# Optimization experiments

Measured on AMD Instinct MI355X. Metric: run time of the kernel, lower is better.

Reference implementation:

```python
import jax, jax.numpy as jnp
import numpy as np

D_IN = 1024
D_OUT = 1024
NUM_HEADS = 16
HEAD_DIM = D_OUT // NUM_HEADS


def setup_inputs() -> dict:
    key = jax.random.key(0)
    k_x, k_q, k_k, k_v, k_o, k_ob = jax.random.split(key, 6)
    s_in = 1.0 / np.sqrt(D_IN)
    s_out = 1.0 / np.sqrt(D_OUT)
    return {
        "x": jax.random.normal(k_x, (4, 2048, D_IN), dtype=jnp.float32),
        "W_Q": jax.random.uniform(k_q, (D_IN, D_OUT), jnp.float32, -s_in, s_in),
        "W_K": jax.random.uniform(k_k, (D_IN, D_OUT), jnp.float32, -s_in, s_in),
        "W_V": jax.random.uniform(k_v, (D_IN, D_OUT), jnp.float32, -s_in, s_in),
        "W_O": jax.random.uniform(k_o, (D_OUT, D_OUT), jnp.float32, -s_out, s_out),
        "b_O": jax.random.uniform(k_ob, (D_OUT,), jnp.float32, -s_out, s_out),
    }


def reference(x, W_Q, W_K, W_V, W_O, b_O):
    B, T, _ = x.shape
    # projections -> [B, H, T, Dh]
    Q = (x @ W_Q).reshape(B, T, NUM_HEADS, HEAD_DIM).transpose(0, 2, 1, 3)
    K = (x @ W_K).reshape(B, T, NUM_HEADS, HEAD_DIM).transpose(0, 2, 1, 3)
    V = (x @ W_V).reshape(B, T, NUM_HEADS, HEAD_DIM).transpose(0, 2, 1, 3)
    scores = jnp.einsum("bhqd,bhkd->bhqk", Q, K) / np.sqrt(HEAD_DIM).astype(np.float32)
    causal = jnp.tril(jnp.ones((T, T), dtype=bool))  # True = keep
    scores = jnp.where(causal, scores, -jnp.inf)
    weights = jax.nn.softmax(scores, axis=-1)
    ctx = jnp.einsum("bhqk,bhkd->bhqd", weights, V)
    ctx = ctx.transpose(0, 2, 1, 3).reshape(B, T, D_OUT)
    return ctx @ W_O + b_O
```

## Files before the change

### kernel.cpp

```cpp
#include <hip/hip_runtime.h>

typedef unsigned short ushort_t;
typedef __attribute__((ext_vector_type(8))) __bf16 bf16x8;
typedef __attribute__((ext_vector_type(4))) float f32x4;
typedef __attribute__((ext_vector_type(16))) float f32x16;
typedef __attribute__((ext_vector_type(4))) unsigned short us4;
typedef __attribute__((ext_vector_type(8))) unsigned short us8;
typedef __attribute__((ext_vector_type(4))) unsigned int u32x4;

#define AS1 __attribute__((address_space(1)))
#define AS3 __attribute__((address_space(3)))

__device__ __forceinline__ unsigned short f2bf(float f) {
    unsigned u = __float_as_uint(f);
    u += 0x7fff + ((u >> 16) & 1);
    return (unsigned short)(u >> 16);
}

__device__ __forceinline__ unsigned cvtpk_bf16(float lo, float hi) {
    unsigned r;
    asm("v_cvt_pk_bf16_f32 %0, %1, %2" : "=v"(r) : "v"(lo), "v"(hi));
    return r;
}

__device__ __forceinline__ float fast_exp2(float x) {
    float r;
    asm("v_exp_f32 %0, %1" : "=v"(r) : "v"(x));
    return r;
}

__global__ void k_convert_x(const float* __restrict__ x, ushort_t* __restrict__ xb, int n4) {
    int i = blockIdx.x * blockDim.x + threadIdx.x;
    int stride = gridDim.x * blockDim.x;
    for (; i < n4; i += stride) {
        float4 f = reinterpret_cast<const float4*>(x)[i];
        us4 o = { f2bf(f.x), f2bf(f.y), f2bf(f.z), f2bf(f.w) };
        reinterpret_cast<us4*>(xb)[i] = o;
    }
}

__global__ void k_transpose_w(const float* __restrict__ wq, const float* __restrict__ wk,
                              const float* __restrict__ wv, const float* __restrict__ wo,
                              ushort_t* __restrict__ wqkvt, ushort_t* __restrict__ wot) {
    __shared__ float t[64][65];
    int bx = blockIdx.x;
    int w = bx >> 8;
    int ti = bx & 255;
    int k0 = (ti >> 4) * 64, n0 = (ti & 15) * 64;
    const float* src = (w == 0) ? wq : (w == 1) ? wk : (w == 2) ? wv : wo;
    ushort_t* dst = (w < 3) ? (wqkvt + (size_t)w * 1048576) : wot;
    for (int i = threadIdx.x; i < 4096; i += 256) {
        int r = i >> 6, c = i & 63;
        t[c][r] = src[(size_t)(k0 + r) * 1024 + n0 + c];
    }
    __syncthreads();
    for (int i = threadIdx.x; i < 4096; i += 256) {
        int r = i >> 6, c = i & 63;
        dst[(size_t)(n0 + r) * 1024 + k0 + c] = f2bf(t[r][c]);
    }
}

__global__ __launch_bounds__(512, 2) void k_gemm_qkv256(
    const ushort_t* __restrict__ A, const ushort_t* __restrict__ Bm,
    ushort_t* __restrict__ qd, ushort_t* __restrict__ kd, ushort_t* __restrict__ vtd) {
    __shared__ __attribute__((aligned(16))) ushort_t lds[2 * 28672];

    const int tid = threadIdx.x, wid = tid >> 6, lane = tid & 63;
    const int lr = lane & 15, lg = lane >> 4;
    const int wm = wid >> 2, wn = wid & 3;

    int bid = blockIdx.x;
    int wg = (bid & 7) * 64 + (bid >> 3);
    const int by = wg >> 4, bx = wg & 15;
    const int row0 = by * 256, col0 = bx * 192;

    const int srcrow = lane >> 2;
    const int srccol = (((lane & 3) * 16) ^ ((lane >> 5) << 5)) >> 1;
    const ushort_t* aS = A  + (size_t)(row0 + srcrow) * 1024 + srccol;
    const ushort_t* bS = Bm + (size_t)(col0 + srcrow) * 1024 + srccol;
    const int rdoff = (lr * 64 + lg * 16) ^ ((lr >> 3) << 5);

    const int s0 = (wid & 3) + ((wid >> 2) << 3);
    const int s1 = s0 + 4;
    const int bmix_sr = 8 + (wid & 3);
    const int bmix_sc = wid >> 2;

#define STG_A(kt, sr, sc) \
    __builtin_amdgcn_global_load_lds((const AS1 void*)(aS + (size_t)(sr) * 16384 + (kt) * 64 + (sc) * 32), \
        (AS3 void*)((AS3 char*)lds + ((kt) & 1) * 57344 + (sr) * 2048 + (sc) * 1024), 16, 0, 0)
#define STG_B(kt, sr, sc) \
    __builtin_amdgcn_global_load_lds((const AS1 void*)(bS + (size_t)(sr) * 16384 + (kt) * 64 + (sc) * 32), \
        (AS3 void*)((AS3 char*)lds + ((kt) & 1) * 57344 + 32768 + (sr) * 2048 + (sc) * 1024), 16, 0, 0)
#define GRP1(kt)  { STG_A(kt, s0, 0); STG_B(kt, wid, 0); }
#define GRP2(kt)  { STG_A(kt, s1, 0); }
#define GRP3(kt)  { STG_A(kt, s0, 1); STG_B(kt, wid, 1); }
#define GTOP(kt)  { STG_A(kt, s1, 1); STG_B(kt, bmix_sr, bmix_sc); }

    f32x4 acc[8][3] = {};

    GRP1(0); GRP2(0); GRP3(0); GTOP(0);
    GRP1(1); GRP2(1); GRP3(1);

#pragma unroll 1
    for (int kt = 0; kt < 16; ++kt) {
        if (kt < 15) asm volatile("s_waitcnt vmcnt(5)" ::: "memory");
        else         asm volatile("s_waitcnt vmcnt(0)" ::: "memory");
        __builtin_amdgcn_s_barrier();
        if (kt < 15) GTOP(kt + 1);

        const char* bufA = (const char*)lds + (kt & 1) * 57344;
        const char* bufB = bufA + 32768;

        bf16x8 av0[4], av1[4], bv0[3], bv1[3];
#pragma unroll
        for (int x = 0; x < 4; ++x)
            av0[x] = *reinterpret_cast<const bf16x8*>(bufA + (wm * 8 + x) * 2048 + rdoff);
#pragma unroll
        for (int x = 0; x < 3; ++x)
            bv0[x] = *reinterpret_cast<const bf16x8*>(bufB + (wn * 3 + x) * 2048 + rdoff);

#pragma unroll
        for (int x = 0; x < 4; ++x)
            av1[x] = *reinterpret_cast<const bf16x8*>(bufA + (wm * 8 + 4 + x) * 2048 + rdoff);
        __builtin_amdgcn_s_setprio(1);
#pragma unroll
        for (int mf = 0; mf < 4; ++mf)
#pragma unroll
            for (int nf = 0; nf < 3; ++nf)
                acc[mf][nf] = __builtin_amdgcn_mfma_f32_16x16x32_bf16(av0[mf], bv0[nf], acc[mf][nf], 0, 0, 0);
        __builtin_amdgcn_s_setprio(0);
        __builtin_amdgcn_s_barrier();

#pragma unroll
        for (int x = 0; x < 4; ++x)
            av0[x] = *reinterpret_cast<const bf16x8*>(bufA + (wm * 8 + x) * 2048 + 1024 + rdoff);
#pragma unroll
        for (int x = 0; x < 3; ++x)
            bv1[x] = *reinterpret_cast<const bf16x8*>(bufB + (wn * 3 + x) * 2048 + 1024 + rdoff);
        __builtin_amdgcn_s_setprio(1);
#pragma unroll
        for (int mf = 0; mf < 4; ++mf)
#pragma unroll
            for (int nf = 0; nf < 3; ++nf)
                acc[4 + mf][nf] = __builtin_amdgcn_mfma_f32_16x16x32_bf16(av1[mf], bv0[nf], acc[4 + mf][nf], 0, 0, 0);
        __builtin_amdgcn_s_setprio(0);
        if (kt < 14) GRP1(kt + 2);
        __builtin_amdgcn_s_barrier();

#pragma unroll
        for (int x = 0; x < 4; ++x)
            av1[x] = *reinterpret_cast<const bf16x8*>(bufA + (wm * 8 + 4 + x) * 2048 + 1024 + rdoff);
        __builtin_amdgcn_s_setprio(1);
#pragma unroll
        for (int mf = 0; mf < 4; ++mf)
#pragma unroll
            for (int nf = 0; nf < 3; ++nf)
                acc[mf][nf] = __builtin_amdgcn_mfma_f32_16x16x32_bf16(av0[mf], bv1[nf], acc[mf][nf], 0, 0, 0);
        __builtin_amdgcn_s_setprio(0);
        if (kt < 14) GRP2(kt + 2);
        __builtin_amdgcn_s_barrier();

        __builtin_amdgcn_s_setprio(1);
#pragma unroll
        for (int mf = 0; mf < 4; ++mf)
#pragma unroll
            for (int nf = 0; nf < 3; ++nf)
                acc[4 + mf][nf] = __builtin_amdgcn_mfma_f32_16x16x32_bf16(av1[mf], bv1[nf], acc[4 + mf][nf], 0, 0, 0);
        __builtin_amdgcn_s_setprio(0);
        if (kt < 14) GRP3(kt + 2);
    }
#undef STG_A
#undef STG_B
#undef GRP1
#undef GRP2
#undef GRP3
#undef GTOP

#pragma unroll
    for (int mi = 0; mi < 8; ++mi) {
#pragma unroll
        for (int nf = 0; nf < 3; ++nf) {
            int col = col0 + wn * 48 + nf * 16 + lr;
            int w = col >> 10;
            int c1 = col & 1023;
            int h = c1 >> 6, dh = c1 & 63;
            if (w < 2) {
                ushort_t* dst = (w == 0) ? qd : kd;
                const float osc = (w == 0) ? 0.18033688f : 1.0f;
#pragma unroll
                for (int e = 0; e < 4; ++e) {
                    int row = row0 + wm * 128 + mi * 16 + lg * 4 + e;
                    int b = row >> 11, t = row & 2047;
                    dst[(((size_t)(b * 16 + h)) * 2048 + t) * 64 + dh] = f2bf(acc[mi][nf][e] * osc);
                }
            } else {
                int rbase = row0 + wm * 128 + mi * 16 + lg * 4;
                int b = rbase >> 11, t0 = rbase & 2047;
                us4 o = { f2bf(acc[mi][nf][0]), f2bf(acc[mi][nf][1]),
                          f2bf(acc[mi][nf][2]), f2bf(acc[mi][nf][3]) };
                *reinterpret_cast<us4*>(
                    &vtd[(((size_t)(b * 16 + h)) * 64 + dh) * 2048 + t0]) = o;
            }
        }
    }
}

__global__ __launch_bounds__(256) void k_attn(
    const ushort_t* __restrict__ q, const ushort_t* __restrict__ k,
    const ushort_t* __restrict__ v, ushort_t* __restrict__ ctx) {
    __shared__ __attribute__((aligned(16))) ushort_t lsK[2 * 8192];
    __shared__ __attribute__((aligned(16))) ushort_t lsV[2 * 8192];

    const int tid = threadIdx.x, wid = tid >> 6, lane = tid & 63;
    const int l31 = lane & 31, hi = lane >> 5;
    const int bid = blockIdx.x;
    const int bh = bid & 63, pi = bid >> 6;
    const size_t base = (size_t)bh * 2048 * 64;
    const ushort_t* qg = q + base;
    const ushort_t* kg = k + base;
    const ushort_t* vtg = v + base;
    const int b = bh >> 4, h = bh & 15;

    const int skey = wid * 8 + (lane >> 3);
    const int scb0 = ((lane & 7) * 16) ^ ((skey & 7) << 4);
    const int kx = (l31 & 7) << 4;
    int koffA[4];
#pragma unroll
    for (int s = 0; s < 4; ++s)
        koffA[s] = l31 * 128 + ((s * 32 + hi * 16) ^ kx);

    us8 ow;
#pragma unroll
    for (int e = 0; e < 8; ++e) ow[e] = 0x3F80;
    const bf16x8 onef = __builtin_bit_cast(bf16x8, ow);

#pragma unroll 1
    for (int pass = 0; pass < 2; ++pass) {
        const int qt = pass ? pi : (15 - pi);
        const int q0 = qt * 128;
        const int q0w = q0 + wid * 32;
        const int qrow = q0w + l31;
        const int njt = qt + 1;

        bf16x8 qf[4];
#pragma unroll
        for (int s = 0; s < 4; ++s)
            qf[s] = *reinterpret_cast<const bf16x8*>(qg + (size_t)qrow * 64 + s * 16 + hi * 8);

        const ushort_t* kpr[4];
        const ushort_t* vpr[4];
#pragma unroll
        for (int r = 0; r < 4; ++r) {
            kpr[r] = kg + (size_t)(r * 32 + skey) * 64 + (scb0 >> 1);
            vpr[r] = vtg + (size_t)((r & 1) * 32 + skey) * 2048 + (r >> 1) * 64 + (scb0 >> 1);
        }

        f32x16 acc0 = {}, acc1 = {}, lacc = {};

        __syncthreads();
#pragma unroll
        for (int r = 0; r < 4; ++r) {
            __builtin_amdgcn_global_load_lds((const AS1 void*)kpr[r],
                (AS3 void*)((AS3 char*)lsK + r * 4096 + wid * 1024), 16, 0, 0);
            __builtin_amdgcn_global_load_lds((const AS1 void*)vpr[r],
                (AS3 void*)((AS3 char*)lsV + r * 4096 + wid * 1024), 16, 0, 0);
        }

        unsigned bo = 0;
        for (int jt = 0; jt < njt; ++jt) {
            __syncthreads();
            const int j0 = jt << 7;
            if (jt + 1 < njt) {
                const unsigned nb = bo ^ 16384;
#pragma unroll
                for (int r = 0; r < 4; ++r) {
                    kpr[r] += 8192;
                    vpr[r] += 128;
                    __builtin_amdgcn_global_load_lds((const AS1 void*)kpr[r],
                        (AS3 void*)((AS3 char*)lsK + nb + r * 4096 + wid * 1024), 16, 0, 0);
                    __builtin_amdgcn_global_load_lds((const AS1 void*)vpr[r],
                        (AS3 void*)((AS3 char*)lsV + nb + r * 4096 + wid * 1024), 16, 0, 0);
                }
            }

#pragma unroll
            for (int hh = 0; hh < 2; ++hh) {
                const int j0h = j0 + hh * 64;
                if (j0h < q0w + 32) {
                    const char* bK = reinterpret_cast<const char*>(lsK) + bo + hh * 8192;
                    const char* bV = reinterpret_cast<const char*>(lsV) + bo + hh * 8192;

                    f32x16 s0 = {}, s1 = {};
#pragma unroll
                    for (int s = 0; s < 4; ++s) {
                        bf16x8 ka = *reinterpret_cast<const bf16x8*>(bK + koffA[s]);
                        s0 = __builtin_amdgcn_mfma_f32_32x32x16_bf16(ka, qf[s], s0, 0, 0, 0);
                    }
#pragma unroll
                    for (int s = 0; s < 4; ++s) {
                        bf16x8 ka = *reinterpret_cast<const bf16x8*>(bK + 4096 + koffA[s]);
                        s1 = __builtin_amdgcn_mfma_f32_32x32x16_bf16(ka, qf[s], s1, 0, 0, 0);
                    }

                    float p0[16], p1[16];
                    if (j0h + 63 > q0w) {
                        const int jh = j0h + 4 * hi;
#pragma unroll
                        for (int r = 0; r < 16; ++r) {
                            const int kl = jh + (r & 3) + 8 * (r >> 2);
                            float e0 = fast_exp2(s0[r]);
                            float e1 = fast_exp2(s1[r]);
                            p0[r] = (kl > qrow) ? 0.f : e0;
                            p1[r] = (kl + 32 > qrow) ? 0.f : e1;
                        }
                    } else {
#pragma unroll
                        for (int r = 0; r < 16; ++r) {
                            p0[r] = fast_exp2(s0[r]);
                            p1[r] = fast_exp2(s1[r]);
                        }
                    }

#pragma unroll
                    for (int kb = 0; kb < 2; ++kb) {
                        const float* pp = kb ? p1 : p0;
                        unsigned pw[8];
#pragma unroll
                        for (int g = 0; g < 4; ++g) {
                            pw[2 * g]     = cvtpk_bf16(pp[4 * g],     pp[4 * g + 1]);
                            pw[2 * g + 1] = cvtpk_bf16(pp[4 * g + 2], pp[4 * g + 3]);
                        }
#pragma unroll
                        for (int j = 0; j < 2; ++j) {
                            asm("v_permlane32_swap_b32 %0, %1" : "+v"(pw[4 * j]),     "+v"(pw[4 * j + 2]));
                            asm("v_permlane32_swap_b32 %0, %1" : "+v"(pw[4 * j + 1]), "+v"(pw[4 * j + 3]));
                            u32x4 fw = { pw[4 * j], pw[4 * j + 1], pw[4 * j + 2], pw[4 * j + 3] };
                            bf16x8 pf = __builtin_bit_cast(bf16x8, fw);
                            const int jj = kb * 2 + j;
                            {
                                bf16x8 vf = *reinterpret_cast<const bf16x8*>(bV + koffA[jj]);
                                acc0 = __builtin_amdgcn_mfma_f32_32x32x16_bf16(vf, pf, acc0, 0, 0, 0);
                            }
                            {
                                bf16x8 vf = *reinterpret_cast<const bf16x8*>(bV + 4096 + koffA[jj]);
                                acc1 = __builtin_amdgcn_mfma_f32_32x32x16_bf16(vf, pf, acc1, 0, 0, 0);
                            }
                            lacc = __builtin_amdgcn_mfma_f32_32x32x16_bf16(onef, pf, lacc, 0, 0, 0);
                        }
                    }
                }
            }
            bo ^= 16384;
        }

        float inv = 1.0f / lacc[0];
        size_t orow = ((size_t)(b * 2048 + qrow)) * 1024 + h * 64;
#pragma unroll
        for (int g = 0; g < 4; ++g) {
            us4 o0 = { f2bf(acc0[4 * g] * inv),     f2bf(acc0[4 * g + 1] * inv),
                       f2bf(acc0[4 * g + 2] * inv), f2bf(acc0[4 * g + 3] * inv) };
            *reinterpret_cast<us4*>(&ctx[orow + 8 * g + 4 * hi]) = o0;
            us4 o1 = { f2bf(acc1[4 * g] * inv),     f2bf(acc1[4 * g + 1] * inv),
                       f2bf(acc1[4 * g + 2] * inv), f2bf(acc1[4 * g + 3] * inv) };
            *reinterpret_cast<us4*>(&ctx[orow + 32 + 8 * g + 4 * hi]) = o1;
        }
    }
}

__global__ __launch_bounds__(256, 2) void k_gemm_out(
    const ushort_t* __restrict__ cb, const ushort_t* __restrict__ wot,
    const float* __restrict__ bO, float* __restrict__ out) {
    __shared__ __attribute__((aligned(16))) ushort_t lds[2 * 16384];

    const int tid = threadIdx.x, wid = tid >> 6, lane = tid & 63;
    const int lr = lane & 15, lg = lane >> 4;
    const int wm = wid >> 1, wn = wid & 1;

    int bid = blockIdx.x;
    int wg = (bid & 7) * 64 + (bid >> 3);
    const int by = wg >> 3, bx = wg & 7;
    const int row0 = by * 128, col0 = bx * 128;

    const int srcrow = lane >> 2;
    const int srccol = (((lane & 3) * 16) ^ ((lane >> 5) << 5)) >> 1;
    const ushort_t* aS = cb  + (size_t)(row0 + srcrow) * 1024 + srccol;
    const ushort_t* bS = wot + (size_t)(col0 + srcrow) * 1024 + srccol;
    const int rdoff = (lr * 64 + lg * 16) ^ ((lr >> 3) << 5);

#define STG_A(kt, sr, sc) \
    __builtin_amdgcn_global_load_lds((const AS1 void*)(aS + (size_t)(sr) * 16384 + (kt) * 64 + (sc) * 32), \
        (AS3 void*)((AS3 char*)lds + ((kt) & 1) * 32768 + (sr) * 2048 + (sc) * 1024), 16, 0, 0)
#define STG_B(kt, sr, sc) \
    __builtin_amdgcn_global_load_lds((const AS1 void*)(bS + (size_t)(sr) * 16384 + (kt) * 64 + (sc) * 32), \
        (AS3 void*)((AS3 char*)lds + ((kt) & 1) * 32768 + 16384 + (sr) * 2048 + (sc) * 1024), 16, 0, 0)
#define GRP1(kt)  { STG_A(kt, wid, 0); STG_A(kt, wid + 4, 0); STG_B(kt, wid, 0); STG_B(kt, wid + 4, 0); }
#define GTOP(kt)  { STG_A(kt, wid, 1); STG_A(kt, wid + 4, 1); STG_B(kt, wid, 1); STG_B(kt, wid + 4, 1); }

    f32x4 acc[4][4] = {};

    GRP1(0); GTOP(0); GRP1(1);

#pragma unroll 1
    for (int kt = 0; kt < 16; ++kt) {
        if (kt < 15) asm volatile("s_waitcnt vmcnt(4)" ::: "memory");
        else         asm volatile("s_waitcnt vmcnt(0)" ::: "memory");
        __builtin_amdgcn_s_barrier();
        if (kt < 15) GTOP(kt + 1);

        const char* bufA = (const char*)lds + (kt & 1) * 32768;
        const char* bufB = bufA + 16384;

        bf16x8 av0[2], av1[2], bv0[4], bv1[4];
#pragma unroll
        for (int x = 0; x < 2; ++x)
            av0[x] = *reinterpret_cast<const bf16x8*>(bufA + (wm * 4 + x) * 2048 + rdoff);
#pragma unroll
        for (int x = 0; x < 4; ++x)
            bv0[x] = *reinterpret_cast<const bf16x8*>(bufB + (wn * 4 + x) * 2048 + rdoff);

#pragma unroll
        for (int x = 0; x < 2; ++x)
            av1[x] = *reinterpret_cast<const bf16x8*>(bufA + (wm * 4 + 2 + x) * 2048 + rdoff);
        __builtin_amdgcn_s_setprio(1);
#pragma unroll
        for (int mf = 0; mf < 2; ++mf)
#pragma unroll
            for (int nf = 0; nf < 4; ++nf)
                acc[mf][nf] = __builtin_amdgcn_mfma_f32_16x16x32_bf16(av0[mf], bv0[nf], acc[mf][nf], 0, 0, 0);
        __builtin_amdgcn_s_setprio(0);
        __builtin_amdgcn_s_barrier();

#pragma unroll
        for (int x = 0; x < 2; ++x)
            av0[x] = *reinterpret_cast<const bf16x8*>(bufA + (wm * 4 + x) * 2048 + 1024 + rdoff);
#pragma unroll
        for (int x = 0; x < 4; ++x)
            bv1[x] = *reinterpret_cast<const bf16x8*>(bufB + (wn * 4 + x) * 2048 + 1024 + rdoff);
        __builtin_amdgcn_s_setprio(1);
#pragma unroll
        for (int mf = 0; mf < 2; ++mf)
#pragma unroll
            for (int nf = 0; nf < 4; ++nf)
                acc[2 + mf][nf] = __builtin_amdgcn_mfma_f32_16x16x32_bf16(av1[mf], bv0[nf], acc[2 + mf][nf], 0, 0, 0);
        __builtin_amdgcn_s_setprio(0);
        if (kt < 14) GRP1(kt + 2);
        __builtin_amdgcn_s_barrier();

#pragma unroll
        for (int x = 0; x < 2; ++x)
            av1[x] = *reinterpret_cast<const bf16x8*>(bufA + (wm * 4 + 2 + x) * 2048 + 1024 + rdoff);
        __builtin_amdgcn_s_setprio(1);
#pragma unroll
        for (int mf = 0; mf < 2; ++mf)
#pragma unroll
            for (int nf = 0; nf < 4; ++nf)
                acc[mf][nf] = __builtin_amdgcn_mfma_f32_16x16x32_bf16(av0[mf], bv1[nf], acc[mf][nf], 0, 0, 0);
        __builtin_amdgcn_s_setprio(0);
        __builtin_amdgcn_s_barrier();

        __builtin_amdgcn_s_setprio(1);
#pragma unroll
        for (int mf = 0; mf < 2; ++mf)
#pragma unroll
            for (int nf = 0; nf < 4; ++nf)
                acc[2 + mf][nf] = __builtin_amdgcn_mfma_f32_16x16x32_bf16(av1[mf], bv1[nf], acc[2 + mf][nf], 0, 0, 0);
        __builtin_amdgcn_s_setprio(0);
    }
#undef STG_A
#undef STG_B
#undef GRP1
#undef GTOP

#pragma unroll
    for (int mf = 0; mf < 4; ++mf) {
#pragma unroll
        for (int nf = 0; nf < 4; ++nf) {
            int col = col0 + wn * 64 + nf * 16 + lr;
            float bias = bO[col];
#pragma unroll
            for (int e = 0; e < 4; ++e) {
                int row = row0 + wm * 64 + mf * 16 + lg * 4 + e;
                out[(size_t)row * 1024 + col] = acc[mf][nf][e] + bias;
            }
        }
    }
}

extern "C" void kernel_launch(void* const* d_in, const int* in_sizes, int n_in,
                              void* d_out, int out_size, void* d_ws, size_t ws_size,
                              hipStream_t stream) {
    const float* x  = (const float*)d_in[0];
    const float* wq = (const float*)d_in[1];
    const float* wk = (const float*)d_in[2];
    const float* wv = (const float*)d_in[3];
    const float* wo = (const float*)d_in[4];
    const float* bo = (const float*)d_in[5];
    float* out = (float*)d_out;

    char* ws = (char*)d_ws;
    ushort_t* xb    = (ushort_t*)(ws);
    ushort_t* wqkvt = (ushort_t*)(ws + 16777216);
    ushort_t* wot   = (ushort_t*)(ws + 23068672);
    ushort_t* qd    = (ushort_t*)(ws + 25165824);
    ushort_t* kd    = (ushort_t*)(ws + 41943040);
    ushort_t* vtd   = (ushort_t*)(ws + 58720256);
    ushort_t* cd    = (ushort_t*)(ws + 75497472);

    k_convert_x<<<2048, 256, 0, stream>>>(x, xb, 8192 * 1024 / 4);
    k_transpose_w<<<1024, 256, 0, stream>>>(wq, wk, wv, wo, wqkvt, wot);
    k_gemm_qkv256<<<512, 512, 0, stream>>>(xb, wqkvt, qd, kd, vtd);
    k_attn<<<512, 256, 0, stream>>>(qd, kd, vtd, cd);
    k_gemm_out<<<dim3(512), 256, 0, stream>>>(cd, wot, bo, out);
}
```

Measured before the change: 152.0 us.

## Shrink QKV GEMM tile to 128x192 and double the grid

The QKV projection GEMM moves from 256x192 tiles on 512 blocks to 128x192 tiles on 1024 blocks. LDS per block shrinks and launch bounds are raised to 4 blocks per CU. The k-loop pipeline becomes two MFMA phases with fewer staging groups and a lower vmcnt wait. The aim is more concurrent blocks and better CU balance, at the cost of lower arithmetic intensity per tile and more global reloads of the weight matrix.

```diff
diff --git a/kernel.cpp b/kernel.cpp
--- a/kernel.cpp
+++ b/kernel.cpp
@@ -60,19 +60,19 @@
     }
 }
 
-__global__ __launch_bounds__(512, 2) void k_gemm_qkv256(
+__global__ __launch_bounds__(512, 4) void k_gemm_qkv128(
     const ushort_t* __restrict__ A, const ushort_t* __restrict__ Bm,
     ushort_t* __restrict__ qd, ushort_t* __restrict__ kd, ushort_t* __restrict__ vtd) {
-    __shared__ __attribute__((aligned(16))) ushort_t lds[2 * 28672];
+    __shared__ __attribute__((aligned(16))) ushort_t lds[2 * 20480];
 
     const int tid = threadIdx.x, wid = tid >> 6, lane = tid & 63;
     const int lr = lane & 15, lg = lane >> 4;
     const int wm = wid >> 2, wn = wid & 3;
 
     int bid = blockIdx.x;
-    int wg = (bid & 7) * 64 + (bid >> 3);
+    int wg = (bid & 7) * 128 + (bid >> 3);
     const int by = wg >> 4, bx = wg & 15;
-    const int row0 = by * 256, col0 = bx * 192;
+    const int row0 = by * 128, col0 = bx * 192;
 
     const int srcrow = lane >> 2;
     const int srccol = (((lane & 3) * 16) ^ ((lane >> 5) << 5)) >> 1;
@@ -80,48 +80,44 @@
     const ushort_t* bS = Bm + (size_t)(col0 + srcrow) * 1024 + srccol;
     const int rdoff = (lr * 64 + lg * 16) ^ ((lr >> 3) << 5);
 
-    const int s0 = (wid & 3) + ((wid >> 2) << 3);
-    const int s1 = s0 + 4;
-    const int bmix_sr = 8 + (wid & 3);
-    const int bmix_sc = wid >> 2;
+    const int bx_sr = 8 + (wid & 3);
+    const int bx_sc = wid >> 2;
 
 #define STG_A(kt, sr, sc) \
     __builtin_amdgcn_global_load_lds((const AS1 void*)(aS + (size_t)(sr) * 16384 + (kt) * 64 + (sc) * 32), \
-        (AS3 void*)((AS3 char*)lds + ((kt) & 1) * 57344 + (sr) * 2048 + (sc) * 1024), 16, 0, 0)
+        (AS3 void*)((AS3 char*)lds + ((kt) & 1) * 40960 + (sr) * 2048 + (sc) * 1024), 16, 0, 0)
 #define STG_B(kt, sr, sc) \
     __builtin_amdgcn_global_load_lds((const AS1 void*)(bS + (size_t)(sr) * 16384 + (kt) * 64 + (sc) * 32), \
-        (AS3 void*)((AS3 char*)lds + ((kt) & 1) * 57344 + 32768 + (sr) * 2048 + (sc) * 1024), 16, 0, 0)
-#define GRP1(kt)  { STG_A(kt, s0, 0); STG_B(kt, wid, 0); }
-#define GRP2(kt)  { STG_A(kt, s1, 0); }
-#define GRP3(kt)  { STG_A(kt, s0, 1); STG_B(kt, wid, 1); }
-#define GTOP(kt)  { STG_A(kt, s1, 1); STG_B(kt, bmix_sr, bmix_sc); }
-
-    f32x4 acc[8][3] = {};
-
-    GRP1(0); GRP2(0); GRP3(0); GTOP(0);
-    GRP1(1); GRP2(1); GRP3(1);
+        (AS3 void*)((AS3 char*)lds + ((kt) & 1) * 40960 + 16384 + (sr) * 2048 + (sc) * 1024), 16, 0, 0)
+#define GTOP(kt)  { STG_A(kt, wid, 1); STG_B(kt, wid, 1); }
+#define GRP1(kt)  { STG_A(kt, wid, 0); STG_B(kt, wid, 0); STG_B(kt, bx_sr, bx_sc); }
+
+    f32x4 acc[4][3] = {};
+
+    GRP1(0); GTOP(0); GRP1(1);
 
 #pragma unroll 1
     for (int kt = 0; kt < 16; ++kt) {
-        if (kt < 15) asm volatile("s_waitcnt vmcnt(5)" ::: "memory");
+        if (kt < 15) asm volatile("s_waitcnt vmcnt(3)" ::: "memory");
         else         asm volatile("s_waitcnt vmcnt(0)" ::: "memory");
         __builtin_amdgcn_s_barrier();
         if (kt < 15) GTOP(kt + 1);
 
-        const char* bufA = (const char*)lds + (kt & 1) * 57344;
-        const char* bufB = bufA + 32768;
+        const char* bufA = (const char*)lds + (kt & 1) * 40960;
+        const char* bufB = bufA + 16384;
 
         bf16x8 av0[4], av1[4], bv0[3], bv1[3];
 #pragma unroll
-        for (int x = 0; x < 4; ++x)
-            av0[x] = *reinterpret_cast<const bf16x8*>(bufA + (wm * 8 + x) * 2048 + rdoff);
-#pragma unroll
-        for (int x = 0; x < 3; ++x)
+        for (int x = 0; x < 4; ++x) {
+            av0[x] = *reinterpret_cast<const bf16x8*>(bufA + (wm * 4 + x) * 2048 + rdoff);
+            av1[x] = *reinterpret_cast<const bf16x8*>(bufA + (wm * 4 + x) * 2048 + 1024 + rdoff);
+        }
+#pragma unroll
+        for (int x = 0; x < 3; ++x) {
             bv0[x] = *reinterpret_cast<const bf16x8*>(bufB + (wn * 3 + x) * 2048 + rdoff);
-
-#pragma unroll
-        for (int x = 0; x < 4; ++x)
-            av1[x] = *reinterpret_cast<const bf16x8*>(bufA + (wm * 8 + 4 + x) * 2048 + rdoff);
+            bv1[x] = *reinterpret_cast<const bf16x8*>(bufB + (wn * 3 + x) * 2048 + 1024 + rdoff);
+        }
+
         __builtin_amdgcn_s_setprio(1);
 #pragma unroll
         for (int mf = 0; mf < 4; ++mf)
@@ -131,53 +127,22 @@
         __builtin_amdgcn_s_setprio(0);
         __builtin_amdgcn_s_barrier();
 
-#pragma unroll
-        for (int x = 0; x < 4; ++x)
-            av0[x] = *reinterpret_cast<const bf16x8*>(bufA + (wm * 8 + x) * 2048 + 1024 + rdoff);
-#pragma unroll
-        for (int x = 0; x < 3; ++x)
-            bv1[x] = *reinterpret_cast<const bf16x8*>(bufB + (wn * 3 + x) * 2048 + 1024 + rdoff);
+        if (kt < 14) GRP1(kt + 2);
         __builtin_amdgcn_s_setprio(1);
 #pragma unroll
         for (int mf = 0; mf < 4; ++mf)
 #pragma unroll
             for (int nf = 0; nf < 3; ++nf)
-                acc[4 + mf][nf] = __builtin_amdgcn_mfma_f32_16x16x32_bf16(av1[mf], bv0[nf], acc[4 + mf][nf], 0, 0, 0);
-        __builtin_amdgcn_s_setprio(0);
-        if (kt < 14) GRP1(kt + 2);
-        __builtin_amdgcn_s_barrier();
-
-#pragma unroll
-        for (int x = 0; x < 4; ++x)
-            av1[x] = *reinterpret_cast<const bf16x8*>(bufA + (wm * 8 + 4 + x) * 2048 + 1024 + rdoff);
-        __builtin_amdgcn_s_setprio(1);
-#pragma unroll
-        for (int mf = 0; mf < 4; ++mf)
-#pragma unroll
-            for (int nf = 0; nf < 3; ++nf)
-                acc[mf][nf] = __builtin_amdgcn_mfma_f32_16x16x32_bf16(av0[mf], bv1[nf], acc[mf][nf], 0, 0, 0);
-        __builtin_amdgcn_s_setprio(0);
-        if (kt < 14) GRP2(kt + 2);
-        __builtin_amdgcn_s_barrier();
-
-        __builtin_amdgcn_s_setprio(1);
-#pragma unroll
-        for (int mf = 0; mf < 4; ++mf)
-#pragma unroll
-            for (int nf = 0; nf < 3; ++nf)
-                acc[4 + mf][nf] = __builtin_amdgcn_mfma_f32_16x16x32_bf16(av1[mf], bv1[nf], acc[4 + mf][nf], 0, 0, 0);
-        __builtin_amdgcn_s_setprio(0);
-        if (kt < 14) GRP3(kt + 2);
+                acc[mf][nf] = __builtin_amdgcn_mfma_f32_16x16x32_bf16(av1[mf], bv1[nf], acc[mf][nf], 0, 0, 0);
+        __builtin_amdgcn_s_setprio(0);
     }
 #undef STG_A
 #undef STG_B
+#undef GTOP
 #undef GRP1
-#undef GRP2
-#undef GRP3
-#undef GTOP
-
-#pragma unroll
-    for (int mi = 0; mi < 8; ++mi) {
+
+#pragma unroll
+    for (int mf = 0; mf < 4; ++mf) {
 #pragma unroll
         for (int nf = 0; nf < 3; ++nf) {
             int col = col0 + wn * 48 + nf * 16 + lr;
@@ -189,15 +154,15 @@
                 const float osc = (w == 0) ? 0.18033688f : 1.0f;
 #pragma unroll
                 for (int e = 0; e < 4; ++e) {
-                    int row = row0 + wm * 128 + mi * 16 + lg * 4 + e;
+                    int row = row0 + wm * 64 + mf * 16 + lg * 4 + e;
                     int b = row >> 11, t = row & 2047;
-                    dst[(((size_t)(b * 16 + h)) * 2048 + t) * 64 + dh] = f2bf(acc[mi][nf][e] * osc);
+                    dst[(((size_t)(b * 16 + h)) * 2048 + t) * 64 + dh] = f2bf(acc[mf][nf][e] * osc);
                 }
             } else {
-                int rbase = row0 + wm * 128 + mi * 16 + lg * 4;
+                int rbase = row0 + wm * 64 + mf * 16 + lg * 4;
                 int b = rbase >> 11, t0 = rbase & 2047;
-                us4 o = { f2bf(acc[mi][nf][0]), f2bf(acc[mi][nf][1]),
-                          f2bf(acc[mi][nf][2]), f2bf(acc[mi][nf][3]) };
+                us4 o = { f2bf(acc[mf][nf][0]), f2bf(acc[mf][nf][1]),
+                          f2bf(acc[mf][nf][2]), f2bf(acc[mf][nf][3]) };
                 *reinterpret_cast<us4*>(
                     &vtd[(((size_t)(b * 16 + h)) * 64 + dh) * 2048 + t0]) = o;
             }
@@ -508,7 +473,7 @@
 
     k_convert_x<<<2048, 256, 0, stream>>>(x, xb, 8192 * 1024 / 4);
     k_transpose_w<<<1024, 256, 0, stream>>>(wq, wk, wv, wo, wqkvt, wot);
-    k_gemm_qkv256<<<512, 512, 0, stream>>>(xb, wqkvt, qd, kd, vtd);
+    k_gemm_qkv128<<<1024, 512, 0, stream>>>(xb, wqkvt, qd, kd, vtd);
     k_attn<<<512, 256, 0, stream>>>(qd, kd, vtd, cd);
     k_gemm_out<<<dim3(512), 256, 0, stream>>>(cd, wot, bo, out);
 }
```

Result: no change. 152.4 us (+0.3%).
